# Kernel optimization log

Hardware: AMD Instinct MI355X
Metric: run time of the kernel (lower is better)

The kernel has to match this reference:

```python
import jax, jax.numpy as jnp
import numpy as np

B, C_CLS, D_WORD, J = 1024, 80, 300, 8000
IMG_CH = 2048

def setup_inputs() -> dict:
    key = jax.random.key(0)
    ks = jax.random.split(key, 9)
    return {
        'feature': jax.random.normal(ks[0], (B, IMG_CH), jnp.float32),
        'inp': jax.random.normal(ks[1], (1, C_CLS, D_WORD), jnp.float32),
        'A': jax.random.uniform(ks[2], (C_CLS, C_CLS), jnp.float32),
        'W_gc1': jax.random.normal(ks[3], (D_WORD, 1024), jnp.float32) * (1.0 / np.sqrt(1024)),
        'W_gc2': jax.random.normal(ks[4], (1024, 2048), jnp.float32) * (1.0 / np.sqrt(2048)),
        'W_img': jax.random.normal(ks[5], (J, IMG_CH), jnp.float32) * 0.02,
        'b_img': jax.random.normal(ks[6], (J,), jnp.float32) * 0.02,
        'W_cls': jax.random.normal(ks[7], (J, 2048), jnp.float32) * 0.02,
        'b_cls': jax.random.normal(ks[8], (J,), jnp.float32) * 0.02,
    }

def _gen_adj(A):
    # torch: D = A.sum(1)**-0.5; adj = (A @ diag(D)).T @ diag(D) = D[:,None]*A.T*D[None,:]
    D = jnp.power(jnp.sum(A, axis=1), -0.5)
    return D[:, None] * A.T * D[None, :]

def reference(feature, inp, A, W_gc1, W_gc2, W_img, b_img, W_cls, b_cls):
    inp0 = inp[0]                                   # [C, 300]
    adj = jax.lax.stop_gradient(_gen_adj(A))        # [C, C], .detach() in torch
    x = adj @ (inp0 @ W_gc1)                        # gc1: [C, 1024]
    x = jax.nn.leaky_relu(x, negative_slope=0.2)
    x = adj @ (x @ W_gc2)                           # gc2: [C, 2048]
    # MFB bilinear pooling (is_usemfb=True, is_hash=False -> out_in_tmp=1, eval-mode dropout=identity)
    # original: out[b,c] = sum_j (Linear_img(feature[b])[j] * Linear_cls(x_col_c)[j])
    img_proj = feature @ W_img.T + b_img            # [B, J]
    cls_proj = x @ W_cls.T + b_cls                  # [C, J]
    x_out = img_proj @ cls_proj.T                   # [B, C]
    return x_out
```

## Files before the change

kernel.cpp:

```cpp
#include <hip/hip_runtime.h>
#include <hip/hip_bf16.h>


typedef __bf16 bf16_t;
typedef __bf16 bf16x8 __attribute__((ext_vector_type(8)));
typedef float f32x4 __attribute__((ext_vector_type(4)));

#define MFMA16(a, b, c) __builtin_amdgcn_mfma_f32_16x16x32_bf16((a), (b), (c), 0, 0, 0)

__device__ inline bf16x8 cvt8(float4 a, float4 b) {
  bf16x8 v;
  v[0] = (bf16_t)a.x; v[1] = (bf16_t)a.y; v[2] = (bf16_t)a.z; v[3] = (bf16_t)a.w;
  v[4] = (bf16_t)b.x; v[5] = (bf16_t)b.y; v[6] = (bf16_t)b.z; v[7] = (bf16_t)b.w;
  return v;
}

__global__ void k_adj(const float* __restrict__ A, float* __restrict__ adj) {
  __shared__ float Dv[80];
  int tid = threadIdx.x;
  if (tid < 80) {
    float s = 0.f;
    #pragma unroll 4
    for (int j = 0; j < 80; ++j) s += A[tid * 80 + j];
    Dv[tid] = rsqrtf(s);
  }
  __syncthreads();
  for (int idx = tid; idx < 6400; idx += blockDim.x) {
    int i = idx / 80, j = idx % 80;
    adj[idx] = Dv[i] * Dv[j] * A[j * 80 + i];
  }
}

__global__ void k_cvt0(const float* __restrict__ inp0, bf16_t* __restrict__ x0b) {
  int idx = blockIdx.x * blockDim.x + threadIdx.x;
  if (idx < 30720) {
    int c = idx / 384, k = idx % 384;
    x0b[idx] = (k < 300) ? (bf16_t)inp0[c * 300 + k] : (bf16_t)0.f;
  }
}

__global__ __launch_bounds__(256) void k_gc1m(
    const bf16_t* __restrict__ x0b, const float* __restrict__ Wgc1,
    float* __restrict__ t1) {
  int tid = threadIdx.x;
  int w = tid >> 6, l = tid & 63;
  int ln = l & 15, q = l >> 4;
  int n0 = blockIdx.x * 16;

  __shared__ float red[4][80][16];
  f32x4 acc[5] = {};
  for (int ks = 0; ks < 3; ++ks) {
    int kq = w * 96 + ks * 32 + q * 8;
    bf16x8 bfrag;
    #pragma unroll
    for (int jj = 0; jj < 8; ++jj) {
      int k = kq + jj;
      int kc = k < 300 ? k : 299;
      float wv = Wgc1[kc * 1024 + n0 + ln];
      bfrag[jj] = (bf16_t)(k < 300 ? wv : 0.f);
    }
    #pragma unroll
    for (int mt = 0; mt < 5; ++mt) {
      bf16x8 afrag = *(const bf16x8*)(x0b + (size_t)(mt * 16 + ln) * 384 + kq);
      acc[mt] = MFMA16(afrag, bfrag, acc[mt]);
    }
  }
  #pragma unroll
  for (int mt = 0; mt < 5; ++mt)
    #pragma unroll
    for (int reg = 0; reg < 4; ++reg)
      red[w][mt * 16 + q * 4 + reg][ln] = acc[mt][reg];
  __syncthreads();
  for (int o = tid; o < 1280; o += 256) {
    int c = o >> 4, nn = o & 15;
    t1[c * 1024 + n0 + nn] = red[0][c][nn] + red[1][c][nn] + red[2][c][nn] + red[3][c][nn];
  }
}

__global__ void k_adjmul_leaky(const float* __restrict__ adj, const float* __restrict__ t1,
                               bf16_t* __restrict__ x1b) {
  int idx = blockIdx.x * blockDim.x + threadIdx.x;
  int c = idx >> 10, n = idx & 1023;
  const float* ar = adj + c * 80;
  float acc = 0.f;
  #pragma unroll 4
  for (int cc = 0; cc < 80; ++cc) acc += ar[cc] * t1[cc * 1024 + n];
  x1b[idx] = (bf16_t)(acc > 0.f ? acc : 0.2f * acc);
}

__global__ __launch_bounds__(256) void k_gc2m(
    const bf16_t* __restrict__ x1b, const float* __restrict__ Wgc2,
    float* __restrict__ t2p) {
  int tid = threadIdx.x;
  int w = tid >> 6, l = tid & 63;
  int ln = l & 15, q = l >> 4;
  int nc = blockIdx.x & 31, kc = blockIdx.x >> 5;
  const float* wbase = Wgc2 + (size_t)(kc * 128) * 2048 + nc * 64;

  __shared__ float Bs[2][32][66];
  float4 pv[2];
  #pragma unroll
  for (int it = 0; it < 2; ++it) {
    int slot = tid + it * 256, kr = slot >> 4, nq = slot & 15;
    pv[it] = *(const float4*)(wbase + (size_t)kr * 2048 + nq * 4);
  }
  f32x4 acc[5] = {};
  for (int s = 0; s < 4; ++s) {
    #pragma unroll
    for (int it = 0; it < 2; ++it) {
      int slot = tid + it * 256, kr = slot >> 4, nq = slot & 15;
      *(float4*)&Bs[s & 1][kr][nq * 4] = pv[it];
    }
    __syncthreads();
    if (s < 3) {
      #pragma unroll
      for (int it = 0; it < 2; ++it) {
        int slot = tid + it * 256, kr = slot >> 4, nq = slot & 15;
        pv[it] = *(const float4*)(wbase + (size_t)((s + 1) * 32 + kr) * 2048 + nq * 4);
      }
    }
    int k0 = kc * 128 + s * 32;
    bf16x8 bfrag;
    #pragma unroll
    for (int jj = 0; jj < 8; ++jj) bfrag[jj] = (bf16_t)Bs[s & 1][q * 8 + jj][w * 16 + ln];
    #pragma unroll
    for (int mt = 0; mt < 5; ++mt) {
      bf16x8 afrag = *(const bf16x8*)(x1b + (size_t)(mt * 16 + ln) * 1024 + k0 + q * 8);
      acc[mt] = MFMA16(afrag, bfrag, acc[mt]);
    }
  }
  float* tp = t2p + (size_t)kc * 163840 + nc * 64 + w * 16 + ln;
  #pragma unroll
  for (int mt = 0; mt < 5; ++mt)
    #pragma unroll
    for (int reg = 0; reg < 4; ++reg)
      tp[(size_t)(mt * 16 + q * 4 + reg) * 2048] = acc[mt][reg];
}

__global__ void k_t2red(const float* __restrict__ t2p, float* __restrict__ t2) {
  int i = blockIdx.x * 256 + threadIdx.x;
  float s = 0.f;
  #pragma unroll
  for (int p = 0; p < 8; ++p) s += t2p[(size_t)p * 163840 + i];
  t2[i] = s;
}

__global__ void k_adjmul_bf16(const float* __restrict__ adj, const float* __restrict__ t2,
                              bf16_t* __restrict__ x2) {
  int idx = blockIdx.x * blockDim.x + threadIdx.x;
  int c = idx >> 11, n = idx & 2047;
  const float* ar = adj + c * 80;
  float acc = 0.f;
  #pragma unroll 4
  for (int cc = 0; cc < 80; ++cc) acc += ar[cc] * t2[cc * 2048 + n];
  x2[idx] = (bf16_t)acc;
}

__global__ __launch_bounds__(512) void k_clsproj(
    const float* __restrict__ Wcls, const float* __restrict__ bcls,
    const float* __restrict__ bimg, const bf16_t* __restrict__ x2,
    bf16_t* __restrict__ P, float* __restrict__ r) {
  int tid = threadIdx.x;
  int w = tid >> 6, l = tid & 63;
  int ln = l & 15, q = l >> 4;
  int j0 = blockIdx.x * 16;
  size_t jrow = (size_t)(j0 + ln) * 2048;

  __shared__ float red[8][80][16];
  __shared__ float rloc[80];
  if (tid < 80) rloc[tid] = 0.f;

  f32x4 acc[5] = {};
  int kbase = w * 256 + q * 8;
  for (int ks = 0; ks < 8; ++ks) {
    int kq = kbase + ks * 32;
    const float4* bp = (const float4*)(Wcls + jrow + kq);
    float4 b0 = bp[0], b1 = bp[1];
    bf16x8 bfrag = cvt8(b0, b1);
    #pragma unroll
    for (int mt = 0; mt < 5; ++mt) {
      bf16x8 afrag = *(const bf16x8*)(x2 + (size_t)(mt * 16 + ln) * 2048 + kq);
      acc[mt] = MFMA16(afrag, bfrag, acc[mt]);
    }
  }
  #pragma unroll
  for (int mt = 0; mt < 5; ++mt)
    #pragma unroll
    for (int reg = 0; reg < 4; ++reg)
      red[w][mt * 16 + q * 4 + reg][ln] = acc[mt][reg];
  __syncthreads();

  for (int o = tid; o < 1280; o += 512) {
    int c = o >> 4, jj = o & 15;
    float v = bcls[j0 + jj];
    #pragma unroll
    for (int ww = 0; ww < 8; ++ww) v += red[ww][c][jj];
    P[(size_t)c * 8000 + j0 + jj] = (bf16_t)v;
    atomicAdd(&rloc[c], bimg[j0 + jj] * v);
  }
  __syncthreads();
  if (tid < 80) atomicAdd(&r[tid], rloc[tid]);
}

__global__ __launch_bounds__(256) void k_hmat(
    const float* __restrict__ Wimg, const bf16_t* __restrict__ P, float* __restrict__ Hp) {
  int tid = threadIdx.x;
  int w = tid >> 6, l = tid & 63;
  int ln = l & 15, q = l >> 4;
  int nc = blockIdx.x & 31, jc = blockIdx.x >> 5;
  const float* wbase = Wimg + (size_t)(jc * 320) * 2048 + nc * 64;

  __shared__ float Bs[2][32][66];
  float4 pv[2];
  #pragma unroll
  for (int it = 0; it < 2; ++it) {
    int slot = tid + it * 256, jr = slot >> 4, nq = slot & 15;
    pv[it] = *(const float4*)(wbase + (size_t)jr * 2048 + nq * 4);
  }
  f32x4 acc[5] = {};
  for (int s = 0; s < 10; ++s) {
    #pragma unroll
    for (int it = 0; it < 2; ++it) {
      int slot = tid + it * 256, jr = slot >> 4, nq = slot & 15;
      *(float4*)&Bs[s & 1][jr][nq * 4] = pv[it];
    }
    __syncthreads();
    if (s < 9) {
      #pragma unroll
      for (int it = 0; it < 2; ++it) {
        int slot = tid + it * 256, jr = slot >> 4, nq = slot & 15;
        pv[it] = *(const float4*)(wbase + (size_t)((s + 1) * 32 + jr) * 2048 + nq * 4);
      }
    }
    int j0 = jc * 320 + s * 32;
    bf16x8 bfrag;
    #pragma unroll
    for (int jj = 0; jj < 8; ++jj) bfrag[jj] = (bf16_t)Bs[s & 1][q * 8 + jj][w * 16 + ln];
    #pragma unroll
    for (int mt = 0; mt < 5; ++mt) {
      bf16x8 afrag = *(const bf16x8*)(P + (size_t)(mt * 16 + ln) * 8000 + j0 + q * 8);
      acc[mt] = MFMA16(afrag, bfrag, acc[mt]);
    }
  }
  float* hp = Hp + (size_t)jc * 163840 + nc * 64 + w * 16 + ln;
  #pragma unroll
  for (int mt = 0; mt < 5; ++mt)
    #pragma unroll
    for (int reg = 0; reg < 4; ++reg)
      hp[(size_t)(mt * 16 + q * 4 + reg) * 2048] = acc[mt][reg];
}

__global__ void k_hred(const float* __restrict__ Hp, float* __restrict__ H) {
  int i = blockIdx.x * 256 + threadIdx.x;
  float s = 0.f;
  #pragma unroll
  for (int p = 0; p < 25; ++p) s += Hp[(size_t)p * 163840 + i];
  H[i] = s;
}

__global__ __launch_bounds__(512) void k_out(
    const float* __restrict__ feat, const float* __restrict__ H,
    const float* __restrict__ r, float* __restrict__ out) {
  int tid = threadIdx.x;
  int w = tid >> 6, l = tid & 63;
  int ln = l & 15, q = l >> 4;
  int m0 = blockIdx.x * 16;
  size_t frow = (size_t)(m0 + ln) * 2048;

  __shared__ float red[8][16][80];
  f32x4 acc[5] = {};
  int kbase = w * 256 + q * 8;
  for (int ks = 0; ks < 8; ++ks) {
    int kq = kbase + ks * 32;
    const float4* ap = (const float4*)(feat + frow + kq);
    bf16x8 afrag = cvt8(ap[0], ap[1]);
    #pragma unroll
    for (int nt = 0; nt < 5; ++nt) {
      const float4* hp = (const float4*)(H + (size_t)(nt * 16 + ln) * 2048 + kq);
      bf16x8 bfrag = cvt8(hp[0], hp[1]);
      acc[nt] = MFMA16(afrag, bfrag, acc[nt]);
    }
  }
  #pragma unroll
  for (int nt = 0; nt < 5; ++nt)
    #pragma unroll
    for (int reg = 0; reg < 4; ++reg)
      red[w][q * 4 + reg][nt * 16 + ln] = acc[nt][reg];
  __syncthreads();
  for (int o = tid; o < 1280; o += 512) {
    int mm = o / 80, c = o % 80;
    float v = r[c];
    #pragma unroll
    for (int ww = 0; ww < 8; ++ww) v += red[ww][mm][c];
    out[(m0 + mm) * 80 + c] = v;
  }
}

extern "C" void kernel_launch(void* const* d_in, const int* in_sizes, int n_in,
                              void* d_out, int out_size, void* d_ws, size_t ws_size,
                              hipStream_t stream) {
  const float* feature = (const float*)d_in[0];
  const float* inp     = (const float*)d_in[1];
  const float* A       = (const float*)d_in[2];
  const float* Wgc1    = (const float*)d_in[3];
  const float* Wgc2    = (const float*)d_in[4];
  const float* Wimg    = (const float*)d_in[5];
  const float* bimg    = (const float*)d_in[6];
  const float* Wcls    = (const float*)d_in[7];
  const float* bcls    = (const float*)d_in[8];
  float* out = (float*)d_out;

  char* ws = (char*)d_ws;
  float*  adj = (float*)(ws + 0);
  float*  t1  = (float*)(ws + 25600);
  bf16_t* x1b = (bf16_t*)(ws + 353280);
  float*  t2  = (float*)(ws + 517120);
  bf16_t* x2  = (bf16_t*)(ws + 1172480);
  bf16_t* P   = (bf16_t*)(ws + 1500160);
  float*  H   = (float*)(ws + 2780160);
  float*  r   = (float*)(ws + 3435520);
  bf16_t* x0b = (bf16_t*)(ws + 3435840);
  float*  t2p = (float*)(ws + 3497280);
  float*  Hp  = (float*)(ws + 8740160);

  hipMemsetAsync(r, 0, 80 * 4, stream);

  k_adj<<<1, 128, 0, stream>>>(A, adj);
  k_cvt0<<<120, 256, 0, stream>>>(inp, x0b);
  k_gc1m<<<64, 256, 0, stream>>>(x0b, Wgc1, t1);
  k_adjmul_leaky<<<320, 256, 0, stream>>>(adj, t1, x1b);
  k_gc2m<<<256, 256, 0, stream>>>(x1b, Wgc2, t2p);
  k_t2red<<<640, 256, 0, stream>>>(t2p, t2);
  k_adjmul_bf16<<<640, 256, 0, stream>>>(adj, t2, x2);
  k_clsproj<<<500, 512, 0, stream>>>(Wcls, bcls, bimg, x2, P, r);
  k_hmat<<<800, 256, 0, stream>>>(Wimg, P, Hp);
  k_hred<<<640, 256, 0, stream>>>(Hp, H);
  k_out<<<64, 512, 0, stream>>>(feature, H, r, out);
}
```

Baseline: 284.4 us.

## Reassociate second adj multiply before gc2, merge setup kernels, preload weights

Uses associativity, adj@(x@W2) = (adj@x)@W2, to apply the second adjacency multiply on the 1024-wide activation before the gc2 GEMM, fusing both adjacency multiplies and the leaky ReLU into one shared-memory kernel. This removes the separate 2048-wide adjacency pass and the t2 intermediate. The adj/convert setup and the memset are folded into one launch, and the clsproj and out kernels now issue all their global loads up front. The trade-off is that k_adj2 runs with only 16 blocks, and rounding now happens at a different point in the computation.

```diff
diff --git a/kernel.cpp b/kernel.cpp
--- a/kernel.cpp
+++ b/kernel.cpp
@@ -15,25 +15,26 @@
   return v;
 }
 
-__global__ void k_adj(const float* __restrict__ A, float* __restrict__ adj) {
-  __shared__ float Dv[80];
-  int tid = threadIdx.x;
-  if (tid < 80) {
-    float s = 0.f;
-    #pragma unroll 4
-    for (int j = 0; j < 80; ++j) s += A[tid * 80 + j];
-    Dv[tid] = rsqrtf(s);
-  }
-  __syncthreads();
-  for (int idx = tid; idx < 6400; idx += blockDim.x) {
-    int i = idx / 80, j = idx % 80;
-    adj[idx] = Dv[i] * Dv[j] * A[j * 80 + i];
-  }
-}
-
-__global__ void k_cvt0(const float* __restrict__ inp0, bf16_t* __restrict__ x0b) {
-  int idx = blockIdx.x * blockDim.x + threadIdx.x;
-  if (idx < 30720) {
+__global__ __launch_bounds__(256) void k_setup(
+    const float* __restrict__ A, const float* __restrict__ inp0,
+    float* __restrict__ adj, float* __restrict__ r, bf16_t* __restrict__ x0b) {
+  int tid = threadIdx.x, bid = blockIdx.x;
+  if (bid == 0) {
+    __shared__ float Dv[80];
+    if (tid < 80) {
+      float s = 0.f;
+      #pragma unroll 4
+      for (int j = 0; j < 80; ++j) s += A[tid * 80 + j];
+      Dv[tid] = rsqrtf(s);
+      r[tid] = 0.f;
+    }
+    __syncthreads();
+    for (int idx = tid; idx < 6400; idx += 256) {
+      int i = idx / 80, j = idx % 80;
+      adj[idx] = Dv[i] * Dv[j] * A[j * 80 + i];
+    }
+  } else {
+    int idx = (bid - 1) * 256 + tid;
     int c = idx / 384, k = idx % 384;
     x0b[idx] = (k < 300) ? (bf16_t)inp0[c * 300 + k] : (bf16_t)0.f;
   }
@@ -77,19 +78,39 @@
   }
 }
 
-__global__ void k_adjmul_leaky(const float* __restrict__ adj, const float* __restrict__ t1,
-                               bf16_t* __restrict__ x1b) {
-  int idx = blockIdx.x * blockDim.x + threadIdx.x;
-  int c = idx >> 10, n = idx & 1023;
-  const float* ar = adj + c * 80;
-  float acc = 0.f;
-  #pragma unroll 4
-  for (int cc = 0; cc < 80; ++cc) acc += ar[cc] * t1[cc * 1024 + n];
-  x1b[idx] = (bf16_t)(acc > 0.f ? acc : 0.2f * acc);
+__global__ __launch_bounds__(256) void k_adj2(
+    const float* __restrict__ adj, const float* __restrict__ t1,
+    bf16_t* __restrict__ y) {
+  int tid = threadIdx.x;
+  int n0 = blockIdx.x * 64;
+  __shared__ float adjS[80][80];
+  __shared__ float aS[80][64];
+  __shared__ float bS[80][64];
+  for (int i = tid; i < 6400; i += 256) adjS[i / 80][i % 80] = adj[i];
+  for (int i = tid; i < 5120; i += 256) {
+    int c = i >> 6, nn = i & 63;
+    aS[c][nn] = t1[c * 1024 + n0 + nn];
+  }
+  __syncthreads();
+  for (int i = tid; i < 5120; i += 256) {
+    int c = i >> 6, nn = i & 63;
+    float s = 0.f;
+    #pragma unroll 4
+    for (int cc = 0; cc < 80; ++cc) s += adjS[c][cc] * aS[cc][nn];
+    bS[c][nn] = s > 0.f ? s : 0.2f * s;
+  }
+  __syncthreads();
+  for (int i = tid; i < 5120; i += 256) {
+    int c = i >> 6, nn = i & 63;
+    float s = 0.f;
+    #pragma unroll 4
+    for (int cc = 0; cc < 80; ++cc) s += adjS[c][cc] * bS[cc][nn];
+    y[c * 1024 + n0 + nn] = (bf16_t)s;
+  }
 }
 
 __global__ __launch_bounds__(256) void k_gc2m(
-    const bf16_t* __restrict__ x1b, const float* __restrict__ Wgc2,
+    const bf16_t* __restrict__ y, const float* __restrict__ Wgc2,
     float* __restrict__ t2p) {
   int tid = threadIdx.x;
   int w = tid >> 6, l = tid & 63;
@@ -125,7 +146,7 @@
     for (int jj = 0; jj < 8; ++jj) bfrag[jj] = (bf16_t)Bs[s & 1][q * 8 + jj][w * 16 + ln];
     #pragma unroll
     for (int mt = 0; mt < 5; ++mt) {
-      bf16x8 afrag = *(const bf16x8*)(x1b + (size_t)(mt * 16 + ln) * 1024 + k0 + q * 8);
+      bf16x8 afrag = *(const bf16x8*)(y + (size_t)(mt * 16 + ln) * 1024 + k0 + q * 8);
       acc[mt] = MFMA16(afrag, bfrag, acc[mt]);
     }
   }
@@ -137,23 +158,12 @@
       tp[(size_t)(mt * 16 + q * 4 + reg) * 2048] = acc[mt][reg];
 }
 
-__global__ void k_t2red(const float* __restrict__ t2p, float* __restrict__ t2) {
+__global__ void k_redcvt(const float* __restrict__ t2p, bf16_t* __restrict__ x2) {
   int i = blockIdx.x * 256 + threadIdx.x;
   float s = 0.f;
   #pragma unroll
   for (int p = 0; p < 8; ++p) s += t2p[(size_t)p * 163840 + i];
-  t2[i] = s;
-}
-
-__global__ void k_adjmul_bf16(const float* __restrict__ adj, const float* __restrict__ t2,
-                              bf16_t* __restrict__ x2) {
-  int idx = blockIdx.x * blockDim.x + threadIdx.x;
-  int c = idx >> 11, n = idx & 2047;
-  const float* ar = adj + c * 80;
-  float acc = 0.f;
-  #pragma unroll 4
-  for (int cc = 0; cc < 80; ++cc) acc += ar[cc] * t2[cc * 2048 + n];
-  x2[idx] = (bf16_t)acc;
+  x2[i] = (bf16_t)s;
 }
 
 __global__ __launch_bounds__(512) void k_clsproj(
@@ -170,13 +180,19 @@
   __shared__ float rloc[80];
   if (tid < 80) rloc[tid] = 0.f;
 
-  f32x4 acc[5] = {};
   int kbase = w * 256 + q * 8;
+  float4 wv[16];
+  #pragma unroll
+  for (int ks = 0; ks < 8; ++ks) {
+    const float4* bp = (const float4*)(Wcls + jrow + kbase + ks * 32);
+    wv[2 * ks] = bp[0];
+    wv[2 * ks + 1] = bp[1];
+  }
+  f32x4 acc[5] = {};
+  #pragma unroll
   for (int ks = 0; ks < 8; ++ks) {
     int kq = kbase + ks * 32;
-    const float4* bp = (const float4*)(Wcls + jrow + kq);
-    float4 b0 = bp[0], b1 = bp[1];
-    bf16x8 bfrag = cvt8(b0, b1);
+    bf16x8 bfrag = cvt8(wv[2 * ks], wv[2 * ks + 1]);
     #pragma unroll
     for (int mt = 0; mt < 5; ++mt) {
       bf16x8 afrag = *(const bf16x8*)(x2 + (size_t)(mt * 16 + ln) * 2048 + kq);
@@ -268,12 +284,19 @@
   size_t frow = (size_t)(m0 + ln) * 2048;
 
   __shared__ float red[8][16][80];
-  f32x4 acc[5] = {};
   int kbase = w * 256 + q * 8;
+  float4 fv[16];
+  #pragma unroll
+  for (int ks = 0; ks < 8; ++ks) {
+    const float4* ap = (const float4*)(feat + frow + kbase + ks * 32);
+    fv[2 * ks] = ap[0];
+    fv[2 * ks + 1] = ap[1];
+  }
+  f32x4 acc[5] = {};
+  #pragma unroll
   for (int ks = 0; ks < 8; ++ks) {
     int kq = kbase + ks * 32;
-    const float4* ap = (const float4*)(feat + frow + kq);
-    bf16x8 afrag = cvt8(ap[0], ap[1]);
+    bf16x8 afrag = cvt8(fv[2 * ks], fv[2 * ks + 1]);
     #pragma unroll
     for (int nt = 0; nt < 5; ++nt) {
       const float4* hp = (const float4*)(H + (size_t)(nt * 16 + ln) * 2048 + kq);
@@ -313,25 +336,20 @@
   char* ws = (char*)d_ws;
   float*  adj = (float*)(ws + 0);
   float*  t1  = (float*)(ws + 25600);
-  bf16_t* x1b = (bf16_t*)(ws + 353280);
-  float*  t2  = (float*)(ws + 517120);
-  bf16_t* x2  = (bf16_t*)(ws + 1172480);
-  bf16_t* P   = (bf16_t*)(ws + 1500160);
-  float*  H   = (float*)(ws + 2780160);
-  float*  r   = (float*)(ws + 3435520);
-  bf16_t* x0b = (bf16_t*)(ws + 3435840);
-  float*  t2p = (float*)(ws + 3497280);
-  float*  Hp  = (float*)(ws + 8740160);
-
-  hipMemsetAsync(r, 0, 80 * 4, stream);
-
-  k_adj<<<1, 128, 0, stream>>>(A, adj);
-  k_cvt0<<<120, 256, 0, stream>>>(inp, x0b);
+  bf16_t* y   = (bf16_t*)(ws + 353280);
+  bf16_t* x2  = (bf16_t*)(ws + 517120);
+  bf16_t* P   = (bf16_t*)(ws + 844800);
+  float*  H   = (float*)(ws + 2124800);
+  float*  r   = (float*)(ws + 2780160);
+  bf16_t* x0b = (bf16_t*)(ws + 2780480);
+  float*  t2p = (float*)(ws + 2841920);
+  float*  Hp  = (float*)(ws + 8084800);
+
+  k_setup<<<121, 256, 0, stream>>>(A, inp, adj, r, x0b);
   k_gc1m<<<64, 256, 0, stream>>>(x0b, Wgc1, t1);
-  k_adjmul_leaky<<<320, 256, 0, stream>>>(adj, t1, x1b);
-  k_gc2m<<<256, 256, 0, stream>>>(x1b, Wgc2, t2p);
-  k_t2red<<<640, 256, 0, stream>>>(t2p, t2);
-  k_adjmul_bf16<<<640, 256, 0, stream>>>(adj, t2, x2);
+  k_adj2<<<16, 256, 0, stream>>>(adj, t1, y);
+  k_gc2m<<<256, 256, 0, stream>>>(y, Wgc2, t2p);
+  k_redcvt<<<640, 256, 0, stream>>>(t2p, x2);
   k_clsproj<<<500, 512, 0, stream>>>(Wcls, bcls, bimg, x2, P, r);
   k_hmat<<<800, 256, 0, stream>>>(Wimg, P, Hp);
   k_hred<<<640, 256, 0, stream>>>(Hp, H);
```

Result: slower. 299.5 us (+5.3%).
